# Performance work log

Measured on AMD Instinct MI355X. Metric: run time of the kernel, lower is better.

The kernel has to match this reference:

```python
import jax, jax.numpy as jnp
from jax import lax
import numpy as np

B, CIN, COUT, S = 2, 64, 128, 12
H1, H2 = CIN * 4, COUT * 4          # MBConv hidden dims (expand_ratio=4)
HEADS = 8
MLP_HID = COUT * 4                   # transformer mlp_ratio=4
EPS = 1e-5


def conv1x1(x, w, b=None):
    # 1x1x1 Conv3d == channel matmul. w: [out, in], x: [B,C,H,W,D]
    y = jnp.einsum('oc,bchwd->bohwd', w, x)
    if b is not None:
        y = y + b[None, :, None, None, None]
    return y


def inorm(x, g, b):
    # InstanceNorm3d(affine=True): per-sample, per-channel over spatial dims
    m = x.mean(axis=(2, 3, 4), keepdims=True)
    v = x.var(axis=(2, 3, 4), keepdims=True)
    return (x - m) * jax.lax.rsqrt(v + EPS) * g[None, :, None, None, None] + b[None, :, None, None, None]


def gnorm(x, g, b, groups):
    Bb, C, H, W, D = x.shape
    xr = x.reshape(Bb, groups, C // groups, H, W, D)
    m = xr.mean(axis=(2, 3, 4, 5), keepdims=True)
    v = xr.var(axis=(2, 3, 4, 5), keepdims=True)
    xr = (xr - m) * jax.lax.rsqrt(v + EPS)
    return xr.reshape(Bb, C, H, W, D) * g[None, :, None, None, None] + b[None, :, None, None, None]


def dwconv3(x, w):
    # depthwise 3x3x3, stride 1, pad 1. w: [C,1,3,3,3]
    return lax.conv_general_dilated(
        x, w, window_strides=(1, 1, 1), padding=[(1, 1)] * 3,
        dimension_numbers=('NCDHW', 'OIDHW', 'NCDHW'),
        feature_group_count=x.shape[1])


def mbconv(x, ew, g1, b1, dw, g2, b2, sw1, sb1, sw2, sb2, pw, g3, b3, use_residual):
    res = x
    h = jax.nn.silu(inorm(conv1x1(x, ew), g1, b1))        # expand 1x1
    h = jax.nn.silu(inorm(dwconv3(h, dw), g2, b2))        # depthwise 3x3x3
    s = h.mean(axis=(2, 3, 4), keepdims=True)             # SE: squeeze
    s = jax.nn.silu(conv1x1(s, sw1, sb1))
    s = jax.nn.sigmoid(conv1x1(s, sw2, sb2))
    h = h * s
    h = inorm(conv1x1(h, pw), g3, b3)                     # project
    return res + h if use_residual else h


def mhsa(x, qkv_w, proj_w, proj_b):
    Bb, C, H, W, D = x.shape
    N = H * W * D
    hd = C // HEADS
    qkv = conv1x1(x, qkv_w).reshape(Bb, 3, HEADS, hd, N)
    qkv = jnp.transpose(qkv, (1, 0, 2, 4, 3))             # [3,B,h,N,hd]
    q, k, v = qkv[0], qkv[1], qkv[2]
    attn = jax.nn.softmax(jnp.einsum('bhnd,bhmd->bhnm', q, k) * (hd ** -0.5), axis=-1)
    out = jnp.einsum('bhnm,bhmd->bhnd', attn, v)          # [B,h,N,hd]
    out = jnp.transpose(out, (0, 1, 3, 2)).reshape(Bb, C, H, W, D)
    return conv1x1(out, proj_w, proj_b)


def transformer_block(x, n1g, n1b, qkv, pw, pb, n2g, n2b, mw1, mb1, mw2, mb2):
    x = x + mhsa(gnorm(x, n1g, n1b, min(32, x.shape[1])), qkv, pw, pb)
    h = gnorm(x, n2g, n2b, min(32, x.shape[1]))
    h = conv1x1(jax.nn.gelu(conv1x1(h, mw1, mb1), approximate=False), mw2, mb2)
    return x + h


def shuffle_attn(x, cw1, cw2, gng, gnb, sw):
    b, c, h, w, d = x.shape
    G = 4
    gc = c // (2 * G)  # group_channels
    x6 = x.reshape(b, G, 2 * gc, h, w, d)
    x0 = x6[:, :, :gc].reshape(b * G, gc, h, w, d)
    x1 = x6[:, :, gc:].reshape(b * G, gc, h, w, d)
    # channel branch
    a = x0.mean(axis=(2, 3, 4), keepdims=True)
    a = conv1x1(jax.nn.silu(conv1x1(a, cw1)), cw2)
    x0 = jax.nn.sigmoid(a) * x0
    # spatial branch: GroupNorm(max(1,gc//8)=2 groups) + 1x1 conv
    sgn = gnorm(x1, gng, gnb, max(1, gc // 8))
    x1 = jax.nn.sigmoid(conv1x1(sgn, sw)) * x1
    out = jnp.concatenate([x0.reshape(b, G * gc, h, w, d), x1.reshape(b, G * gc, h, w, d)], axis=1)
    # channel shuffle
    out = out.reshape(b, G, 2 * gc, h, w, d).transpose(0, 2, 1, 3, 4, 5).reshape(b, c, h, w, d)
    return out


def setup_inputs() -> dict:
    key = jax.random.key(0)
    ks = iter(jax.random.split(key, 64))
    w = lambda *shape: jax.random.normal(next(ks), shape, jnp.float32) * 0.05
    p = {}
    p['x'] = jax.random.normal(next(ks), (B, CIN, S, S, S), jnp.float32)
    # mbconv1 (in=64 -> hidden=256 -> out=128), SE reduced = 256//4 = 64
    r1 = H1 // 4
    p['m1_ew'] = w(H1, CIN); p['m1_g1'] = jnp.ones(H1); p['m1_b1'] = jnp.zeros(H1)
    p['m1_dw'] = w(H1, 1, 3, 3, 3); p['m1_g2'] = jnp.ones(H1); p['m1_b2'] = jnp.zeros(H1)
    p['m1_sw1'] = w(r1, H1); p['m1_sb1'] = jnp.zeros(r1)
    p['m1_sw2'] = w(H1, r1); p['m1_sb2'] = jnp.zeros(H1)
    p['m1_pw'] = w(COUT, H1); p['m1_g3'] = jnp.ones(COUT); p['m1_b3'] = jnp.zeros(COUT)
    # mbconv2 (in=128 -> hidden=512 -> out=128, residual), SE reduced = 512//4 = 128
    r2 = H2 // 4
    p['m2_ew'] = w(H2, COUT); p['m2_g1'] = jnp.ones(H2); p['m2_b1'] = jnp.zeros(H2)
    p['m2_dw'] = w(H2, 1, 3, 3, 3); p['m2_g2'] = jnp.ones(H2); p['m2_b2'] = jnp.zeros(H2)
    p['m2_sw1'] = w(r2, H2); p['m2_sb1'] = jnp.zeros(r2)
    p['m2_sw2'] = w(H2, r2); p['m2_sb2'] = jnp.zeros(H2)
    p['m2_pw'] = w(COUT, H2); p['m2_g3'] = jnp.ones(COUT); p['m2_b3'] = jnp.zeros(COUT)
    # transformer
    p['t_n1g'] = jnp.ones(COUT); p['t_n1b'] = jnp.zeros(COUT)
    p['t_qkv'] = w(3 * COUT, COUT)
    p['t_pw'] = w(COUT, COUT); p['t_pb'] = jnp.zeros(COUT)
    p['t_n2g'] = jnp.ones(COUT); p['t_n2b'] = jnp.zeros(COUT)
    p['t_mw1'] = w(MLP_HID, COUT); p['t_mb1'] = jnp.zeros(MLP_HID)
    p['t_mw2'] = w(COUT, MLP_HID); p['t_mb2'] = jnp.zeros(COUT)
    # shuffle attention: group_channels = 128 // 8 = 16, channel_fc reduces to 4
    gc = COUT // 8
    p['s_cw1'] = w(max(1, gc // 4), gc); p['s_cw2'] = w(gc, max(1, gc // 4))
    p['s_gng'] = jnp.ones(gc); p['s_gnb'] = jnp.zeros(gc)
    p['s_sw'] = w(gc, gc)
    return p


def reference(x, m1_ew, m1_g1, m1_b1, m1_dw, m1_g2, m1_b2, m1_sw1, m1_sb1, m1_sw2, m1_sb2, m1_pw, m1_g3, m1_b3, m2_ew, m2_g1, m2_b1, m2_dw, m2_g2, m2_b2, m2_sw1, m2_sb1, m2_sw2, m2_sb2, m2_pw, m2_g3, m2_b3, t_n1g, t_n1b, t_qkv, t_pw, t_pb, t_n2g, t_n2b, t_mw1, t_mb1, t_mw2, t_mb2, s_cw1, s_cw2, s_gng, s_gnb, s_sw):
    x = mbconv(x, m1_ew, m1_g1, m1_b1, m1_dw, m1_g2, m1_b2, m1_sw1, m1_sb1, m1_sw2, m1_sb2, m1_pw, m1_g3, m1_b3, use_residual=False)
    x = mbconv(x, m2_ew, m2_g1, m2_b1, m2_dw, m2_g2, m2_b2, m2_sw1, m2_sb1, m2_sw2, m2_sb2, m2_pw, m2_g3, m2_b3, use_residual=True)
    x = transformer_block(x, t_n1g, t_n1b, t_qkv, t_pw, t_pb, t_n2g, t_n2b, t_mw1, t_mb1, t_mw2, t_mb2)
    x = shuffle_attn(x, s_cw1, s_cw2, s_gng, s_gnb, s_sw)
    return x
```

## Files before the change

### kernel.cpp

```cpp
#include <hip/hip_runtime.h>
#include <cmath>

#define NSP 1728
#define BB  2
#define SS  12

typedef __attribute__((ext_vector_type(8))) short short8;
typedef __attribute__((ext_vector_type(4))) short short4v;
typedef __attribute__((ext_vector_type(4))) float floatx4;

__device__ __forceinline__ short f2bf(float f) {
    unsigned u = __float_as_uint(f);
    u += 0x7fff + ((u >> 16) & 1);
    return (short)(u >> 16);
}
__device__ __forceinline__ unsigned pack2bf(float a, float b) {
    unsigned ua = __float_as_uint(a); ua += 0x7fff + ((ua >> 16) & 1);
    unsigned ub = __float_as_uint(b); ub += 0x7fff + ((ub >> 16) & 1);
    return (ua >> 16) | (ub & 0xffff0000u);
}
__device__ __forceinline__ short8 ld8(const short* p) {
    short4v a = *(const short4v*)p;
    short4v b = *(const short4v*)(p + 4);
    return __builtin_shufflevector(a, b, 0, 1, 2, 3, 4, 5, 6, 7);
}
__device__ __forceinline__ float fexp2(float x) {
    float r;
    asm("v_exp_f32 %0, %1" : "=v"(r) : "v"(x));
    return r;
}

__device__ __forceinline__ void block_reduce2(float& s, float& s2) {
    __shared__ float red[8][2];
    __syncthreads();
    #pragma unroll
    for (int o = 32; o; o >>= 1) {
        s  += __shfl_down(s,  o, 64);
        s2 += __shfl_down(s2, o, 64);
    }
    int lane = threadIdx.x & 63, w = threadIdx.x >> 6;
    if (lane == 0) { red[w][0] = s; red[w][1] = s2; }
    __syncthreads();
    int nw = (blockDim.x + 63) >> 6;
    if (threadIdx.x == 0) {
        float a = 0.f, b = 0.f;
        for (int i = 0; i < nw; i++) { a += red[i][0]; b += red[i][1]; }
        red[0][0] = a; red[0][1] = b;
    }
    __syncthreads();
    s = red[0][0]; s2 = red[0][1];
}

#define WTOT 376832
__global__ __launch_bounds__(256) void prep_kernel(
        const float* __restrict__ s0, const float* __restrict__ s1,
        const float* __restrict__ s2, const float* __restrict__ s3,
        const float* __restrict__ s4, const float* __restrict__ s5,
        const float* __restrict__ s6, const float* __restrict__ s7,
        short* __restrict__ dst, float* __restrict__ stz,
        const float* __restrict__ w1a, const float* __restrict__ w2a,
        const float* __restrict__ w1b, const float* __restrict__ w2b,
        float* __restrict__ tsw) {
    if (blockIdx.x < 11) stz[blockIdx.x * 256 + threadIdx.x] = 0.f;
    if (blockIdx.x >= 368) {
        int e = (blockIdx.x - 368) * 1024 + threadIdx.x * 4;
        #pragma unroll
        for (int k = 0; k < 4; k++) {
            int idx = e + k;
            float v;
            if (idx < 16384) {
                int c = idx >> 6, r = idx & 63;
                v = w1a[r * 256 + c];
            } else if (idx < 32768) {
                int l = idx - 16384; int r = l >> 8, ci = l & 255;
                v = w2a[ci * 64 + r];
            } else if (idx < 98304) {
                int l = idx - 32768; int c = l >> 7, r = l & 127;
                v = w1b[r * 512 + c];
            } else {
                int l = idx - 98304; int r = l >> 9, ci = l & 511;
                v = w2b[ci * 128 + r];
            }
            tsw[idx] = v;
        }
        return;
    }
    const int offs[9] = {0, 16384, 49152, 114688, 180224, 229376, 245760, 311296, WTOT};
    const float* srcs[8] = {s0, s1, s2, s3, s4, s5, s6, s7};
    int e = blockIdx.x * 1024 + threadIdx.x * 4;
    #pragma unroll
    for (int k = 0; k < 4; k++) {
        int idx = e + k;
        int seg = 0;
        while (idx >= offs[seg + 1]) seg++;
        dst[idx] = f2bf(srcs[seg][idx - offs[seg]]);
    }
}

template<int CIN, int COUT>
__global__ __launch_bounds__(256) void convm_kernel(
        const float* __restrict__ in, const short* __restrict__ wb,
        const float* __restrict__ biasc,
        const float* __restrict__ se_s,
        const float* __restrict__ sw1, const float* __restrict__ sb1,
        const float* __restrict__ sw2, const float* __restrict__ sb2, int seR,
        const float* __restrict__ fstats, const float* __restrict__ fg,
        const float* __restrict__ fb, int fgs,
        const float* __restrict__ ing, const float* __restrict__ inb,
        const float* __restrict__ inres,
        const float* __restrict__ po, const float* __restrict__ pl,
        float* __restrict__ xout,
        const float* resid, float* out, float* stats_out,
        const float* __restrict__ statres, int act) {
    constexpr int XP = CIN + 8;
    __shared__ float sc[CIN];
    __shared__ float sh[CIN];
    __shared__ float sa[CIN];
    __shared__ float sbl[CIN];
    __shared__ float hid[128];
    __shared__ __align__(16) short xa[16 * XP];
    int flat = blockIdx.x;
    int b = flat / 108, mt = flat % 108;
    int n0 = mt * 16;
    int tid = threadIdx.x;

    if (po) {
        if (tid < 128) {
            int hh = tid >> 4, j = tid & 15;
            float l = 0.f;
            #pragma unroll
            for (int js = 0; js < 6; js++)
                l += pl[(size_t)((b * 8 + hh) * 6 + js) * NSP + n0 + j];
            hid[tid] = 1.f / l;
        }
        __syncthreads();
        #pragma unroll
        for (int i = 0; i < CIN / 64; i++) {
            int e = tid + i * 256;
            int ci = e >> 2;
            int jj = (e & 3) * 4;
            int hh = ci >> 4, d = ci & 15;
            float4 acc = {0.f, 0.f, 0.f, 0.f};
            #pragma unroll
            for (int js = 0; js < 6; js++) {
                float4 pv = *(const float4*)(po +
                    ((size_t)((b * 8 + hh) * 6 + js) * 16 + d) * NSP + n0 + jj);
                acc.x += pv.x; acc.y += pv.y; acc.z += pv.z; acc.w += pv.w;
            }
            float4 li = *(const float4*)(hid + hh * 16 + jj);
            xa[(jj + 0) * XP + ci] = f2bf(acc.x * li.x);
            xa[(jj + 1) * XP + ci] = f2bf(acc.y * li.y);
            xa[(jj + 2) * XP + ci] = f2bf(acc.z * li.z);
            xa[(jj + 3) * XP + ci] = f2bf(acc.w * li.w);
        }
        __syncthreads();
    } else {
    if (sw1) {
        for (int c = tid; c < CIN; c += 256) { sc[c] = se_s[b * CIN + c]; sh[c] = 0.f; }
        __syncthreads();
        for (int r = tid; r < seR; r += 256) {
            float h0 = sb1[r], h1 = 0.f, h2 = 0.f, h3 = 0.f;
            for (int c = 0; c < CIN; c += 4) {
                h0 = fmaf(sw1[(c + 0) * seR + r], sc[c],     h0);
                h1 = fmaf(sw1[(c + 1) * seR + r], sc[c + 1], h1);
                h2 = fmaf(sw1[(c + 2) * seR + r], sc[c + 2], h2);
                h3 = fmaf(sw1[(c + 3) * seR + r], sc[c + 3], h3);
            }
            float hv = (h0 + h1) + (h2 + h3);
            hid[r] = hv / (1.f + __expf(-hv));
        }
        __syncthreads();
        for (int ci = tid; ci < CIN; ci += 256) {
            float g0 = sb2[ci], g1 = 0.f, g2 = 0.f, g3 = 0.f;
            for (int r = 0; r < seR; r += 4) {
                g0 = fmaf(sw2[(r + 0) * CIN + ci], hid[r],     g0);
                g1 = fmaf(sw2[(r + 1) * CIN + ci], hid[r + 1], g1);
                g2 = fmaf(sw2[(r + 2) * CIN + ci], hid[r + 2], g2);
                g3 = fmaf(sw2[(r + 3) * CIN + ci], hid[r + 3], g3);
            }
            float gv = (g0 + g1) + (g2 + g3);
            sc[ci] = 1.f / (1.f + __expf(-gv));
        }
    } else if (ing) {
        for (int c = tid; c < CIN; c += 256) {
            const float* S = fstats + (size_t)(b * CIN + c) * 5;
            float A = S[0], Bq = S[1], Cq = S[2], Dq = S[3], Eq = S[4];
            const float N = (float)NSP;
            float mean = A / N, var = Bq / N - mean * mean;
            float a_ = ing[c] * rsqrtf(var + 1e-5f);
            float b_ = inb[c] - mean * a_;
            sa[c] = a_; sbl[c] = b_;
            sc[c] = a_ * A + b_ * N + Dq;
            sh[c] = a_ * a_ * Bq + 2.f * a_ * b_ * A + b_ * b_ * N
                  + 2.f * a_ * Cq + 2.f * b_ * Dq + Eq;
        }
        __syncthreads();
        float gS = 0.f, gS2 = 0.f;
        if (tid < CIN) {
            int g0 = (tid / fgs) * fgs;
            for (int k = 0; k < fgs; k++) { gS += sc[g0 + k]; gS2 += sh[g0 + k]; }
        }
        __syncthreads();
        if (tid < CIN) {
            float Ng = fgs * (float)NSP;
            float gm = gS / Ng, gv = gS2 / Ng - gm * gm;
            float s_ = rsqrtf(gv + 1e-5f) * fg[tid];
            sc[tid] = s_;
            sh[tid] = fb[tid] - gm * s_;
        }
    } else if (fstats) {
        for (int c = tid; c < CIN; c += 256) {
            int g0 = c / fgs;
            float S = 0.f, S2 = 0.f;
            for (int k = 0; k < fgs; k++) {
                S  += fstats[(b * CIN + g0 * fgs + k) * 2];
                S2 += fstats[(b * CIN + g0 * fgs + k) * 2 + 1];
            }
            float N = fgs * (float)NSP;
            float mean = S / N, var = S2 / N - mean * mean;
            float s = rsqrtf(var + 1e-5f) * fg[c];
            sc[c] = s;
            sh[c] = fb[c] - mean * s;
        }
    } else {
        for (int c = tid; c < CIN; c += 256) { sc[c] = 1.f; sh[c] = 0.f; }
    }
    __syncthreads();

    bool dosw = (xout != nullptr) && (blockIdx.y == 0);
    #pragma unroll
    for (int i = 0; i < CIN / 64; i++) {
        int e = tid + i * 256;
        int ci = e >> 2;
        int jj = (e & 3) * 4;
        size_t gi = ((size_t)b * CIN + ci) * NSP + n0 + jj;
        float4 v4 = *(const float4*)(in + gi);
        float v0, v1, v2, v3;
        if (ing) {
            float4 rr = *(const float4*)(inres + gi);
            float a_ = sa[ci], b_ = sbl[ci];
            float x0 = fmaf(v4.x, a_, b_) + rr.x;
            float x1 = fmaf(v4.y, a_, b_) + rr.y;
            float x2 = fmaf(v4.z, a_, b_) + rr.z;
            float x3 = fmaf(v4.w, a_, b_) + rr.w;
            if (dosw) {
                float4 o; o.x = x0; o.y = x1; o.z = x2; o.w = x3;
                *(float4*)(xout + gi) = o;
            }
            float s_ = sc[ci], h_ = sh[ci];
            v0 = fmaf(x0, s_, h_); v1 = fmaf(x1, s_, h_);
            v2 = fmaf(x2, s_, h_); v3 = fmaf(x3, s_, h_);
        } else {
            float s_ = sc[ci], h_ = sh[ci];
            v0 = fmaf(v4.x, s_, h_); v1 = fmaf(v4.y, s_, h_);
            v2 = fmaf(v4.z, s_, h_); v3 = fmaf(v4.w, s_, h_);
            if (dosw) {
                float4 o; o.x = v0; o.y = v1; o.z = v2; o.w = v3;
                *(float4*)(xout + gi) = o;
            }
        }
        xa[(jj + 0) * XP + ci] = f2bf(v0);
        xa[(jj + 1) * XP + ci] = f2bf(v1);
        xa[(jj + 2) * XP + ci] = f2bf(v2);
        xa[(jj + 3) * XP + ci] = f2bf(v3);
    }
    __syncthreads();
    }

    int lane = tid & 63, wv = tid >> 6;
    int col = lane & 15, quad = lane >> 4;
    short8 afr[CIN / 32];
    #pragma unroll
    for (int kc = 0; kc < CIN / 32; kc++)
        afr[kc] = ld8(xa + col * XP + kc * 32 + quad * 8);

    int cobase = blockIdx.y * 64 + wv * 16;
    int co = cobase + col;
    const short* wrow = wb + (size_t)co * CIN;
    floatx4 acc = {0.f, 0.f, 0.f, 0.f};
    #pragma unroll
    for (int kc = 0; kc < CIN / 32; kc++) {
        short8 bw = ld8(wrow + kc * 32 + quad * 8);
        acc = __builtin_amdgcn_mfma_f32_16x16x32_bf16(afr[kc], bw, acc, 0, 0, 0);
    }
    float bv = biasc ? biasc[co] : 0.f;
    float r0 = acc[0] + bv, r1 = acc[1] + bv, r2 = acc[2] + bv, r3 = acc[3] + bv;
    if (act == 2) {
        r0 = 0.5f * r0 * (1.f + erff(r0 * 0.70710678118654752f));
        r1 = 0.5f * r1 * (1.f + erff(r1 * 0.70710678118654752f));
        r2 = 0.5f * r2 * (1.f + erff(r2 * 0.70710678118654752f));
        r3 = 0.5f * r3 * (1.f + erff(r3 * 0.70710678118654752f));
    }
    size_t oi = ((size_t)b * COUT + co) * NSP + n0 + quad * 4;
    if (resid) {
        float4 rv = *(const float4*)(resid + oi);
        r0 += rv.x; r1 += rv.y; r2 += rv.z; r3 += rv.w;
    }
    float4 ov; ov.x = r0; ov.y = r1; ov.z = r2; ov.w = r3;
    *(float4*)(out + oi) = ov;
    if (stats_out) {
        if (statres) {
            float4 rv = *(const float4*)(statres + oi);
            float s   = (r0 + r1) + (r2 + r3);
            float s2  = (r0 * r0 + r1 * r1) + (r2 * r2 + r3 * r3);
            float sx  = (r0 * rv.x + r1 * rv.y) + (r2 * rv.z + r3 * rv.w);
            float sr  = (rv.x + rv.y) + (rv.z + rv.w);
            float sr2 = (rv.x * rv.x + rv.y * rv.y) + (rv.z * rv.z + rv.w * rv.w);
            s   += __shfl_xor(s,   16, 64); s   += __shfl_xor(s,   32, 64);
            s2  += __shfl_xor(s2,  16, 64); s2  += __shfl_xor(s2,  32, 64);
            sx  += __shfl_xor(sx,  16, 64); sx  += __shfl_xor(sx,  32, 64);
            sr  += __shfl_xor(sr,  16, 64); sr  += __shfl_xor(sr,  32, 64);
            sr2 += __shfl_xor(sr2, 16, 64); sr2 += __shfl_xor(sr2, 32, 64);
            if (lane < 16) {
                float* sp = stats_out + (size_t)(b * COUT + cobase + lane) * 5;
                atomicAdd(sp + 0, s);
                atomicAdd(sp + 1, s2);
                atomicAdd(sp + 2, sx);
                atomicAdd(sp + 3, sr);
                atomicAdd(sp + 4, sr2);
            }
        } else {
            float s  = (r0 + r1) + (r2 + r3);
            float s2 = (r0 * r0 + r1 * r1) + (r2 * r2 + r3 * r3);
            s  += __shfl_xor(s,  16, 64);
            s  += __shfl_xor(s,  32, 64);
            s2 += __shfl_xor(s2, 16, 64);
            s2 += __shfl_xor(s2, 32, 64);
            if (lane < 16) {
                atomicAdd(&stats_out[(b * COUT + cobase + lane) * 2],     s);
                atomicAdd(&stats_out[(b * COUT + cobase + lane) * 2 + 1], s2);
            }
        }
    }
}

__global__ __launch_bounds__(256) void indw_kernel(
        const float* __restrict__ in,
        const float* __restrict__ g1, const float* __restrict__ b1,
        const float* __restrict__ dw,
        const float* __restrict__ g2, const float* __restrict__ b2,
        float* __restrict__ out, float* __restrict__ se_s, int C) {
    int bc = blockIdx.x;
    int c  = bc % C;
    __shared__ float tile[14 * 14 * 14];
    __shared__ float wsh[27];
    const float* ip = in + (size_t)bc * NSP;
    float r[7];
    float s = 0.f, s2 = 0.f;
    for (int i = threadIdx.x; i < 2744; i += 256) tile[i] = 0.f;
    #pragma unroll
    for (int i = 0; i < 7; i++) {
        int n = threadIdx.x + i * 256;
        if (n < NSP) { r[i] = ip[n]; s += r[i]; s2 += r[i] * r[i]; }
        else r[i] = 0.f;
    }
    if (threadIdx.x < 27) wsh[threadIdx.x] = dw[(size_t)c * 27 + threadIdx.x];
    block_reduce2(s, s2);
    float mean = s / NSP, var = s2 / NSP - (s / NSP) * (s / NSP);
    float rstd = rsqrtf(var + 1e-5f);
    float gc = g1[c], bc1 = b1[c];
    #pragma unroll
    for (int i = 0; i < 7; i++) {
        int n = threadIdx.x + i * 256;
        if (n < NSP) {
            int z = n / 144, y = (n / 12) % 12, x = n % 12;
            float v = (r[i] - mean) * rstd * gc + bc1;
            tile[((z + 1) * 14 + y + 1) * 14 + x + 1] = v / (1.f + __expf(-v));
        }
    }
    __syncthreads();
    float d[7];
    #pragma unroll
    for (int i = 0; i < 7; i++) {
        int n = threadIdx.x + i * 256;
        d[i] = 0.f;
        if (n < NSP) {
            int z = n / 144, y = (n / 12) % 12, x = n % 12;
            const float* ctr = tile + ((z + 1) * 14 + y + 1) * 14 + x + 1;
            float acc = 0.f;
            #pragma unroll
            for (int dz = 0; dz < 3; dz++)
                #pragma unroll
                for (int dy = 0; dy < 3; dy++)
                    #pragma unroll
                    for (int dx = 0; dx < 3; dx++)
                        acc = fmaf(wsh[dz * 9 + dy * 3 + dx],
                                   ctr[(dz - 1) * 196 + (dy - 1) * 14 + (dx - 1)], acc);
            d[i] = acc;
        }
    }
    s = 0.f; s2 = 0.f;
    #pragma unroll
    for (int i = 0; i < 7; i++) {
        int n = threadIdx.x + i * 256;
        if (n < NSP) { s += d[i]; s2 += d[i] * d[i]; }
    }
    block_reduce2(s, s2);
    mean = s / NSP; var = s2 / NSP - mean * mean;
    rstd = rsqrtf(var + 1e-5f);
    float gc2 = g2[c], bc2 = b2[c];
    float ssum = 0.f;
    float* op = out + (size_t)bc * NSP;
    #pragma unroll
    for (int i = 0; i < 7; i++) {
        int n = threadIdx.x + i * 256;
        if (n < NSP) {
            float v = (d[i] - mean) * rstd * gc2 + bc2;
            v = v / (1.f + __expf(-v));
            op[n] = v;
            ssum += v;
        }
    }
    float dummy = 0.f;
    block_reduce2(ssum, dummy);
    if (threadIdx.x == 0) se_s[bc] = ssum / NSP;
}

#define AKT 20
#define AVT 296
#define APT 36
#define JCH 288
__global__ __launch_bounds__(256) void attn_split_kernel(const float* __restrict__ qkv,
                                                         float* __restrict__ po,
                                                         float* __restrict__ pl) {
    __shared__ __align__(16) short kt[JCH * AKT];
    __shared__ __align__(16) short vt[16 * AVT];
    __shared__ __align__(16) short pt[4][16 * APT];
    int bh = blockIdx.x;
    int b = bh >> 3, h = bh & 7;
    int js = blockIdx.z;
    int j0 = js * JCH;
    const float* base = qkv + (size_t)b * 384 * NSP;
    const float* qp = base + (size_t)(h * 16) * NSP;
    const float* kp = base + (size_t)(128 + h * 16) * NSP;
    const float* vp = base + (size_t)(256 + h * 16) * NSP;
    for (int t = threadIdx.x; t < 16 * 144; t += 256) {
        int d = t / 144, j = (t - d * 144) * 2;
        float2 kv2 = *(const float2*)(kp + (size_t)d * NSP + j0 + j);
        float2 vv2 = *(const float2*)(vp + (size_t)d * NSP + j0 + j);
        kt[j * AKT + d]       = f2bf(kv2.x);
        kt[(j + 1) * AKT + d] = f2bf(kv2.y);
        *(unsigned*)(vt + d * AVT + j) = pack2bf(vv2.x, vv2.y);
    }
    int wave = threadIdx.x >> 6, lane = threadIdx.x & 63;
    int m = lane & 15, quad = lane >> 4;
    int q0 = (blockIdx.y * 4 + wave) * 16;
    short* ptw = pt[wave];
    short8 qa;
    #pragma unroll
    for (int i = 0; i < 8; i++) qa[i] = 0;
    if (quad < 2) {
        #pragma unroll
        for (int i = 0; i < 8; i++) {
            int d = quad * 8 + i;
            qa[i] = f2bf(qp[(size_t)d * NSP + q0 + m] * 0.36067376022224085f);
        }
    }
    __syncthreads();
    floatx4 o = {0.f, 0.f, 0.f, 0.f};
    float ls = 0.f;
    for (int s = 0; s < 9; s++) {
        int jl = s * 32;
        short8 ak0, ak1;
        #pragma unroll
        for (int i = 0; i < 8; i++) { ak0[i] = 0; ak1[i] = 0; }
        if (quad < 2) {
            ak0 = ld8(kt + (jl + m) * AKT + quad * 8);
            ak1 = ld8(kt + (jl + 16 + m) * AKT + quad * 8);
        }
        floatx4 s0 = {0.f, 0.f, 0.f, 0.f}, s1 = {0.f, 0.f, 0.f, 0.f};
        s0 = __builtin_amdgcn_mfma_f32_16x16x32_bf16(ak0, qa, s0, 0, 0, 0);
        s1 = __builtin_amdgcn_mfma_f32_16x16x32_bf16(ak1, qa, s1, 0, 0, 0);
        float p0r0 = fexp2(s0[0]), p0r1 = fexp2(s0[1]), p0r2 = fexp2(s0[2]), p0r3 = fexp2(s0[3]);
        float p1r0 = fexp2(s1[0]), p1r1 = fexp2(s1[1]), p1r2 = fexp2(s1[2]), p1r3 = fexp2(s1[3]);
        ls += (p0r0 + p0r1) + (p0r2 + p0r3) + (p1r0 + p1r1) + (p1r2 + p1r3);
        uint2 w0, w1;
        w0.x = pack2bf(p0r0, p0r1); w0.y = pack2bf(p0r2, p0r3);
        w1.x = pack2bf(p1r0, p1r1); w1.y = pack2bf(p1r2, p1r3);
        *(uint2*)(ptw + m * APT + quad * 4)      = w0;
        *(uint2*)(ptw + m * APT + 16 + quad * 4) = w1;
        short8 av = ld8(vt + m * AVT + jl + quad * 8);
        short8 pb = ld8(ptw + m * APT + quad * 8);
        o = __builtin_amdgcn_mfma_f32_16x16x32_bf16(av, pb, o, 0, 0, 0);
    }
    ls += __shfl_xor(ls, 16, 64);
    ls += __shfl_xor(ls, 32, 64);
    size_t pbase = ((size_t)(bh * 6 + js) * 16) * NSP;
    #pragma unroll
    for (int r = 0; r < 4; r++)
        po[pbase + (size_t)(quad * 4 + r) * NSP + q0 + m] = o[r];
    if (quad == 0) pl[(size_t)(bh * 6 + js) * NSP + q0 + m] = ls;
}

__global__ void sfinal_kernel(const float* __restrict__ X,
                              const float* __restrict__ st,
                              const float* __restrict__ cw1,
                              const float* __restrict__ cw2,
                              const float* __restrict__ gng,
                              const float* __restrict__ gnb,
                              const float* __restrict__ sw,
                              float* __restrict__ out) {
    int bg = blockIdx.x;
    int b = bg >> 2, g = bg & 3;
    __shared__ float swl[256];
    for (int i = threadIdx.x; i < 256; i += 64) swl[i] = sw[i];
    __syncthreads();
    float pooled[16];
    #pragma unroll
    for (int j = 0; j < 16; j++)
        pooled[j] = st[(b * 128 + g * 32 + j) * 2] * (1.f / NSP);
    float hid[4];
    #pragma unroll
    for (int r = 0; r < 4; r++) {
        float a = 0.f;
        #pragma unroll
        for (int j = 0; j < 16; j++) a = fmaf(cw1[r * 16 + j], pooled[j], a);
        hid[r] = a / (1.f + __expf(-a));
    }
    float gate[16];
    #pragma unroll
    for (int j = 0; j < 16; j++) {
        float a = 0.f;
        #pragma unroll
        for (int r = 0; r < 4; r++) a = fmaf(cw2[j * 4 + r], hid[r], a);
        gate[j] = 1.f / (1.f + __expf(-a));
    }
    float gmean[2], grstd[2];
    #pragma unroll
    for (int t = 0; t < 2; t++) {
        float S = 0.f, S2 = 0.f;
        #pragma unroll
        for (int k = 0; k < 8; k++) {
            int c = g * 32 + 16 + t * 8 + k;
            S  += st[(b * 128 + c) * 2];
            S2 += st[(b * 128 + c) * 2 + 1];
        }
        float N = 8.f * NSP;
        gmean[t] = S / N;
        grstd[t] = rsqrtf(S2 / N - gmean[t] * gmean[t] + 1e-5f);
    }
    int n = blockIdx.y * 64 + threadIdx.x;
    const float* xb = X + (size_t)b * 128 * NSP;
    #pragma unroll
    for (int j = 0; j < 16; j++) {
        float v = xb[(size_t)(g * 32 + j) * NSP + n] * gate[j];
        int k = g * 16 + j;
        int cp = (k % 32) * 4 + (k / 32);
        out[((size_t)b * 128 + cp) * NSP + n] = v;
    }
    float sgn[16];
    #pragma unroll
    for (int j = 0; j < 16; j++) {
        int grp = j >> 3;
        float xv = xb[(size_t)(g * 32 + 16 + j) * NSP + n];
        sgn[j] = (xv - gmean[grp]) * grstd[grp] * gng[j] + gnb[j];
    }
    #pragma unroll
    for (int j = 0; j < 16; j++) {
        float a = 0.f;
        #pragma unroll
        for (int jp = 0; jp < 16; jp++) a = fmaf(swl[j * 16 + jp], sgn[jp], a);
        float v = (1.f / (1.f + __expf(-a))) * xb[(size_t)(g * 32 + 16 + j) * NSP + n];
        int k = 64 + g * 16 + j;
        int cp = (k % 32) * 4 + (k / 32);
        out[((size_t)b * 128 + cp) * NSP + n] = v;
    }
}

extern "C" void kernel_launch(void* const* d_in, const int* in_sizes, int n_in,
                              void* d_out, int out_size, void* d_ws, size_t ws_size,
                              hipStream_t stream) {
    const float* x     = (const float*)d_in[0];
    const float* m1_ew = (const float*)d_in[1];
    const float* m1_g1 = (const float*)d_in[2];
    const float* m1_b1 = (const float*)d_in[3];
    const float* m1_dw = (const float*)d_in[4];
    const float* m1_g2 = (const float*)d_in[5];
    const float* m1_b2 = (const float*)d_in[6];
    const float* m1_sw1= (const float*)d_in[7];
    const float* m1_sb1= (const float*)d_in[8];
    const float* m1_sw2= (const float*)d_in[9];
    const float* m1_sb2= (const float*)d_in[10];
    const float* m1_pw = (const float*)d_in[11];
    const float* m1_g3 = (const float*)d_in[12];
    const float* m1_b3 = (const float*)d_in[13];
    const float* m2_ew = (const float*)d_in[14];
    const float* m2_g1 = (const float*)d_in[15];
    const float* m2_b1 = (const float*)d_in[16];
    const float* m2_dw = (const float*)d_in[17];
    const float* m2_g2 = (const float*)d_in[18];
    const float* m2_b2 = (const float*)d_in[19];
    const float* m2_sw1= (const float*)d_in[20];
    const float* m2_sb1= (const float*)d_in[21];
    const float* m2_sw2= (const float*)d_in[22];
    const float* m2_sb2= (const float*)d_in[23];
    const float* m2_pw = (const float*)d_in[24];
    const float* m2_g3 = (const float*)d_in[25];
    const float* m2_b3 = (const float*)d_in[26];
    const float* t_n1g = (const float*)d_in[27];
    const float* t_n1b = (const float*)d_in[28];
    const float* t_qkv = (const float*)d_in[29];
    const float* t_pw  = (const float*)d_in[30];
    const float* t_pb  = (const float*)d_in[31];
    const float* t_n2g = (const float*)d_in[32];
    const float* t_n2b = (const float*)d_in[33];
    const float* t_mw1 = (const float*)d_in[34];
    const float* t_mb1 = (const float*)d_in[35];
    const float* t_mw2 = (const float*)d_in[36];
    const float* t_mb2 = (const float*)d_in[37];
    const float* s_cw1 = (const float*)d_in[38];
    const float* s_cw2 = (const float*)d_in[39];
    const float* s_gng = (const float*)d_in[40];
    const float* s_gnb = (const float*)d_in[41];
    const float* s_sw  = (const float*)d_in[42];

    float* out = (float*)d_out;

    float* ws = (float*)d_ws;
    float* bufA   = ws;
    float* bufB   = bufA + (size_t)BB * 512 * NSP;
    float* bufX   = bufB + (size_t)BB * 512 * NSP;
    float* bufY   = bufX + (size_t)BB * 128 * NSP;
    float* bufQKV = bufY + (size_t)BB * 128 * NSP;
    float* pl     = bufQKV + (size_t)BB * 384 * NSP;
    float* small  = pl + (size_t)16 * 6 * NSP;
    float* se_s   = small;
    float* st1    = small + 1024;
    float* st3    = small + 1536;
    float* st4    = small + 2048;
    float* st2    = small + 2560;
    short* wbf    = (short*)(small + 8192);
    float* tsw    = small + 196608;
    float* T_M1SW1 = tsw;
    float* T_M1SW2 = tsw + 16384;
    float* T_M2SW1 = tsw + 32768;
    float* T_M2SW2 = tsw + 98304;
    float* bufX2  = tsw + 163840;
    float* po     = bufA;

    short* W_M1EW = wbf + 0;
    short* W_M1PW = wbf + 16384;
    short* W_M2EW = wbf + 49152;
    short* W_M2PW = wbf + 114688;
    short* W_QKV  = wbf + 180224;
    short* W_TPW  = wbf + 229376;
    short* W_MW1  = wbf + 245760;
    short* W_MW2  = wbf + 311296;

    dim3 blk(256);

    prep_kernel<<<528, blk, 0, stream>>>(
        m1_ew, m1_pw, m2_ew, m2_pw, t_qkv, t_pw, t_mw1, t_mw2, wbf, st1,
        m1_sw1, m1_sw2, m2_sw1, m2_sw2, tsw);

    convm_kernel<64, 256><<<dim3(BB * 108, 4), blk, 0, stream>>>(
        x, W_M1EW, nullptr,
        nullptr, nullptr, nullptr, nullptr, nullptr, 0,
        nullptr, nullptr, nullptr, 0,
        nullptr, nullptr, nullptr,
        nullptr, nullptr, nullptr,
        nullptr, bufA, nullptr, nullptr, 0);
    indw_kernel<<<BB * 256, blk, 0, stream>>>(bufA, m1_g1, m1_b1, m1_dw, m1_g2, m1_b2, bufB, se_s, 256);
    convm_kernel<256, 128><<<dim3(BB * 108, 2), blk, 0, stream>>>(
        bufB, W_M1PW, nullptr,
        se_s, T_M1SW1, m1_sb1, T_M1SW2, m1_sb2, 64,
        nullptr, nullptr, nullptr, 0,
        nullptr, nullptr, nullptr,
        nullptr, nullptr, nullptr,
        nullptr, bufY, st1, nullptr, 0);

    convm_kernel<128, 512><<<dim3(BB * 108, 8), blk, 0, stream>>>(
        bufY, W_M2EW, nullptr,
        nullptr, nullptr, nullptr, nullptr, nullptr, 0,
        st1, m1_g3, m1_b3, 1,
        nullptr, nullptr, nullptr,
        nullptr, nullptr, bufX,
        nullptr, bufA, nullptr, nullptr, 0);
    indw_kernel<<<BB * 512, blk, 0, stream>>>(bufA, m2_g1, m2_b1, m2_dw, m2_g2, m2_b2, bufB, se_s, 512);
    convm_kernel<512, 128><<<dim3(BB * 108, 2), blk, 0, stream>>>(
        bufB, W_M2PW, nullptr,
        se_s, T_M2SW1, m2_sb1, T_M2SW2, m2_sb2, 128,
        nullptr, nullptr, nullptr, 0,
        nullptr, nullptr, nullptr,
        nullptr, nullptr, nullptr,
        nullptr, bufY, st2, bufX, 0);

    convm_kernel<128, 384><<<dim3(BB * 108, 6), blk, 0, stream>>>(
        bufY, W_QKV, nullptr,
        nullptr, nullptr, nullptr, nullptr, nullptr, 0,
        st2, t_n1g, t_n1b, 4,
        m2_g3, m2_b3, bufX,
        nullptr, nullptr, bufX2,
        nullptr, bufQKV, nullptr, nullptr, 0);
    attn_split_kernel<<<dim3(16, 27, 6), blk, 0, stream>>>(bufQKV, po, pl);
    convm_kernel<128, 128><<<dim3(BB * 108, 2), blk, 0, stream>>>(
        nullptr, W_TPW, t_pb,
        nullptr, nullptr, nullptr, nullptr, nullptr, 0,
        nullptr, nullptr, nullptr, 0,
        nullptr, nullptr, nullptr,
        po, pl, nullptr,
        bufX2, bufX2, st3, nullptr, 0);
    convm_kernel<128, 512><<<dim3(BB * 108, 8), blk, 0, stream>>>(
        bufX2, W_MW1, t_mb1,
        nullptr, nullptr, nullptr, nullptr, nullptr, 0,
        st3, t_n2g, t_n2b, 4,
        nullptr, nullptr, nullptr,
        nullptr, nullptr, nullptr,
        nullptr, bufA, nullptr, nullptr, 2);
    convm_kernel<512, 128><<<dim3(BB * 108, 2), blk, 0, stream>>>(
        bufA, W_MW2, t_mb2,
        nullptr, nullptr, nullptr, nullptr, nullptr, 0,
        nullptr, nullptr, nullptr, 0,
        nullptr, nullptr, nullptr,
        nullptr, nullptr, nullptr,
        bufX2, bufX2, st4, nullptr, 0);

    sfinal_kernel<<<dim3(BB * 4, 27), dim3(64), 0, stream>>>(
        bufX2, st4, s_cw1, s_cw2, s_gng, s_gnb, s_sw, out);
}
```

Measured before the change: 333.8 us.

## Fuse all pipeline stages into one cooperative persistent megakernel with grid syncs

Replaces the sequence of about a dozen kernel launches with a single cooperative kernel. Each stage (weight prep, conv matmuls, depthwise conv, attention, final shuffle) becomes a device function looped over work units, with grid-wide syncs between stages and a shared-memory union. The SE gate MLP is moved out of the per-block conv prologue into its own stage that writes the gate once per batch. The aim is to remove launch overhead and the SE work repeated in every block. In exchange, grid syncs cost time, a union sized for the largest stage lowers occupancy, and the grid is capped by occupancy, which may under-parallelise large stages.

```diff
diff --git a/kernel.cpp b/kernel.cpp
--- a/kernel.cpp
+++ b/kernel.cpp
@@ -1,5 +1,8 @@
 #include <hip/hip_runtime.h>
+#include <hip/hip_cooperative_groups.h>
 #include <cmath>
+
+namespace cg = cooperative_groups;
 
 #define NSP 1728
 #define BB  2
@@ -29,6 +32,28 @@
     asm("v_exp_f32 %0, %1" : "=v"(r) : "v"(x));
     return r;
 }
+
+union SMemU {
+    struct {
+        float sc[512], sh[512], sa[512], sbl[512], hid[128];
+        short xa[16 * 520];
+    } conv;
+    struct {
+        float tile[14 * 14 * 14];
+        float wsh[27];
+    } dwc;
+    struct {
+        short kt[288 * 20];
+        short vt[16 * 296];
+        short pt[4][16 * 36];
+    } attn;
+    struct {
+        float pooled[512], hid[128];
+    } seg;
+    struct {
+        float swl[256];
+    } sf;
+};
 
 __device__ __forceinline__ void block_reduce2(float& s, float& s2) {
     __shared__ float red[8][2];
@@ -51,59 +76,99 @@
     s = red[0][0]; s2 = red[0][1];
 }
 
+struct MegaParams {
+    const float *x;
+    const float *m1_g1, *m1_b1, *m1_dw, *m1_g2, *m1_b2, *m1_sb1, *m1_sb2, *m1_g3, *m1_b3;
+    const float *m2_g1, *m2_b1, *m2_dw, *m2_g2, *m2_b2, *m2_sb1, *m2_sb2, *m2_g3, *m2_b3;
+    const float *t_n1g, *t_n1b, *t_pb, *t_n2g, *t_n2b, *t_mb1, *t_mb2;
+    const float *s_cw1, *s_cw2, *s_gng, *s_gnb, *s_sw;
+    const float *pw0, *pw1, *pw2, *pw3, *pw4, *pw5, *pw6, *pw7;
+    const float *sew1a, *sew2a, *sew1b, *sew2b;
+    float *bufA, *bufB, *bufX, *bufY, *bufQKV, *pl;
+    float *se_s, *st1, *st3, *st4, *st2, *gate1, *gate2;
+    short *wbf;
+    float *tsw, *bufX2;
+    float *out;
+};
+
 #define WTOT 376832
-__global__ __launch_bounds__(256) void prep_kernel(
-        const float* __restrict__ s0, const float* __restrict__ s1,
-        const float* __restrict__ s2, const float* __restrict__ s3,
-        const float* __restrict__ s4, const float* __restrict__ s5,
-        const float* __restrict__ s6, const float* __restrict__ s7,
-        short* __restrict__ dst, float* __restrict__ stz,
-        const float* __restrict__ w1a, const float* __restrict__ w2a,
-        const float* __restrict__ w1b, const float* __restrict__ w2b,
-        float* __restrict__ tsw) {
-    if (blockIdx.x < 11) stz[blockIdx.x * 256 + threadIdx.x] = 0.f;
-    if (blockIdx.x >= 368) {
-        int e = (blockIdx.x - 368) * 1024 + threadIdx.x * 4;
+__device__ __forceinline__ void prep_dev(int u, const MegaParams& p) {
+    if (u < 11) p.st1[u * 256 + threadIdx.x] = 0.f;
+    if (u >= 368) {
+        int e = (u - 368) * 1024 + threadIdx.x * 4;
         #pragma unroll
         for (int k = 0; k < 4; k++) {
             int idx = e + k;
             float v;
             if (idx < 16384) {
                 int c = idx >> 6, r = idx & 63;
-                v = w1a[r * 256 + c];
+                v = p.sew1a[r * 256 + c];
             } else if (idx < 32768) {
                 int l = idx - 16384; int r = l >> 8, ci = l & 255;
-                v = w2a[ci * 64 + r];
+                v = p.sew2a[ci * 64 + r];
             } else if (idx < 98304) {
                 int l = idx - 32768; int c = l >> 7, r = l & 127;
-                v = w1b[r * 512 + c];
+                v = p.sew1b[r * 512 + c];
             } else {
                 int l = idx - 98304; int r = l >> 9, ci = l & 511;
-                v = w2b[ci * 128 + r];
-            }
-            tsw[idx] = v;
+                v = p.sew2b[ci * 128 + r];
+            }
+            p.tsw[idx] = v;
         }
         return;
     }
     const int offs[9] = {0, 16384, 49152, 114688, 180224, 229376, 245760, 311296, WTOT};
-    const float* srcs[8] = {s0, s1, s2, s3, s4, s5, s6, s7};
-    int e = blockIdx.x * 1024 + threadIdx.x * 4;
+    const float* srcs[8] = {p.pw0, p.pw1, p.pw2, p.pw3, p.pw4, p.pw5, p.pw6, p.pw7};
+    int e = u * 1024 + threadIdx.x * 4;
     #pragma unroll
     for (int k = 0; k < 4; k++) {
         int idx = e + k;
         int seg = 0;
         while (idx >= offs[seg + 1]) seg++;
-        dst[idx] = f2bf(srcs[seg][idx - offs[seg]]);
+        p.wbf[idx] = f2bf(srcs[seg][idx - offs[seg]]);
+    }
+}
+
+template<int CIN, int SER>
+__device__ __forceinline__ void segate_dev(SMemU& sm, int b,
+        const float* __restrict__ pooled_in,
+        const float* __restrict__ w1t, const float* __restrict__ b1,
+        const float* __restrict__ w2t, const float* __restrict__ b2,
+        float* __restrict__ gate) {
+    int tid = threadIdx.x;
+    __syncthreads();
+    for (int c = tid; c < CIN; c += 256) sm.seg.pooled[c] = pooled_in[b * CIN + c];
+    __syncthreads();
+    if (tid < SER) {
+        float a0 = 0.f, a1 = 0.f, a2 = 0.f, a3 = 0.f;
+        for (int c = 0; c < CIN; c += 4) {
+            a0 = fmaf(w1t[(size_t)(c + 0) * SER + tid], sm.seg.pooled[c + 0], a0);
+            a1 = fmaf(w1t[(size_t)(c + 1) * SER + tid], sm.seg.pooled[c + 1], a1);
+            a2 = fmaf(w1t[(size_t)(c + 2) * SER + tid], sm.seg.pooled[c + 2], a2);
+            a3 = fmaf(w1t[(size_t)(c + 3) * SER + tid], sm.seg.pooled[c + 3], a3);
+        }
+        float h = b1[tid] + (a0 + a1) + (a2 + a3);
+        sm.seg.hid[tid] = h / (1.f + __expf(-h));
+    }
+    __syncthreads();
+    for (int ci = tid; ci < CIN; ci += 256) {
+        float g0 = b2[ci], g1 = 0.f, g2 = 0.f, g3 = 0.f;
+        for (int r = 0; r < SER; r += 4) {
+            g0 = fmaf(w2t[(size_t)(r + 0) * CIN + ci], sm.seg.hid[r + 0], g0);
+            g1 = fmaf(w2t[(size_t)(r + 1) * CIN + ci], sm.seg.hid[r + 1], g1);
+            g2 = fmaf(w2t[(size_t)(r + 2) * CIN + ci], sm.seg.hid[r + 2], g2);
+            g3 = fmaf(w2t[(size_t)(r + 3) * CIN + ci], sm.seg.hid[r + 3], g3);
+        }
+        float gv = (g0 + g1) + (g2 + g3);
+        gate[b * CIN + ci] = 1.f / (1.f + __expf(-gv));
     }
 }
 
 template<int CIN, int COUT>
-__global__ __launch_bounds__(256) void convm_kernel(
+__device__ __forceinline__ void convm_dev(SMemU& sm, int flat, int coy,
         const float* __restrict__ in, const short* __restrict__ wb,
         const float* __restrict__ biasc,
-        const float* __restrict__ se_s,
-        const float* __restrict__ sw1, const float* __restrict__ sb1,
-        const float* __restrict__ sw2, const float* __restrict__ sb2, int seR,
+        const float* __restrict__ segate,
         const float* __restrict__ fstats, const float* __restrict__ fg,
         const float* __restrict__ fb, int fgs,
         const float* __restrict__ ing, const float* __restrict__ inb,
@@ -113,16 +178,16 @@
         const float* resid, float* out, float* stats_out,
         const float* __restrict__ statres, int act) {
     constexpr int XP = CIN + 8;
-    __shared__ float sc[CIN];
-    __shared__ float sh[CIN];
-    __shared__ float sa[CIN];
-    __shared__ float sbl[CIN];
-    __shared__ float hid[128];
-    __shared__ __align__(16) short xa[16 * XP];
-    int flat = blockIdx.x;
+    float* sc  = sm.conv.sc;
+    float* sh  = sm.conv.sh;
+    float* sa  = sm.conv.sa;
+    float* sbl = sm.conv.sbl;
+    float* hid = sm.conv.hid;
+    short* xa  = sm.conv.xa;
     int b = flat / 108, mt = flat % 108;
     int n0 = mt * 16;
     int tid = threadIdx.x;
+    __syncthreads();
 
     if (po) {
         if (tid < 128) {
@@ -155,116 +220,95 @@
         }
         __syncthreads();
     } else {
-    if (sw1) {
-        for (int c = tid; c < CIN; c += 256) { sc[c] = se_s[b * CIN + c]; sh[c] = 0.f; }
+        if (segate) {
+            for (int c = tid; c < CIN; c += 256) {
+                sc[c] = segate[b * CIN + c];
+                sh[c] = 0.f;
+            }
+        } else if (ing) {
+            for (int c = tid; c < CIN; c += 256) {
+                const float* S = fstats + (size_t)(b * CIN + c) * 5;
+                float A = S[0], Bq = S[1], Cq = S[2], Dq = S[3], Eq = S[4];
+                const float N = (float)NSP;
+                float mean = A / N, var = Bq / N - mean * mean;
+                float a_ = ing[c] * rsqrtf(var + 1e-5f);
+                float b_ = inb[c] - mean * a_;
+                sa[c] = a_; sbl[c] = b_;
+                sc[c] = a_ * A + b_ * N + Dq;
+                sh[c] = a_ * a_ * Bq + 2.f * a_ * b_ * A + b_ * b_ * N
+                      + 2.f * a_ * Cq + 2.f * b_ * Dq + Eq;
+            }
+            __syncthreads();
+            float gS = 0.f, gS2 = 0.f;
+            if (tid < CIN) {
+                int g0 = (tid / fgs) * fgs;
+                for (int k = 0; k < fgs; k++) { gS += sc[g0 + k]; gS2 += sh[g0 + k]; }
+            }
+            __syncthreads();
+            if (tid < CIN) {
+                float Ng = fgs * (float)NSP;
+                float gm = gS / Ng, gv = gS2 / Ng - gm * gm;
+                float s_ = rsqrtf(gv + 1e-5f) * fg[tid];
+                sc[tid] = s_;
+                sh[tid] = fb[tid] - gm * s_;
+            }
+        } else if (fstats) {
+            for (int c = tid; c < CIN; c += 256) {
+                int g0 = c / fgs;
+                float S = 0.f, S2 = 0.f;
+                for (int k = 0; k < fgs; k++) {
+                    S  += fstats[(b * CIN + g0 * fgs + k) * 2];
+                    S2 += fstats[(b * CIN + g0 * fgs + k) * 2 + 1];
+                }
+                float N = fgs * (float)NSP;
+                float mean = S / N, var = S2 / N - mean * mean;
+                float s = rsqrtf(var + 1e-5f) * fg[c];
+                sc[c] = s;
+                sh[c] = fb[c] - mean * s;
+            }
+        } else {
+            for (int c = tid; c < CIN; c += 256) { sc[c] = 1.f; sh[c] = 0.f; }
+        }
         __syncthreads();
-        for (int r = tid; r < seR; r += 256) {
-            float h0 = sb1[r], h1 = 0.f, h2 = 0.f, h3 = 0.f;
-            for (int c = 0; c < CIN; c += 4) {
-                h0 = fmaf(sw1[(c + 0) * seR + r], sc[c],     h0);
-                h1 = fmaf(sw1[(c + 1) * seR + r], sc[c + 1], h1);
-                h2 = fmaf(sw1[(c + 2) * seR + r], sc[c + 2], h2);
-                h3 = fmaf(sw1[(c + 3) * seR + r], sc[c + 3], h3);
-            }
-            float hv = (h0 + h1) + (h2 + h3);
-            hid[r] = hv / (1.f + __expf(-hv));
+
+        bool dosw = (xout != nullptr) && (coy == 0);
+        #pragma unroll
+        for (int i = 0; i < CIN / 64; i++) {
+            int e = tid + i * 256;
+            int ci = e >> 2;
+            int jj = (e & 3) * 4;
+            size_t gi = ((size_t)b * CIN + ci) * NSP + n0 + jj;
+            float4 v4 = *(const float4*)(in + gi);
+            float v0, v1, v2, v3;
+            if (ing) {
+                float4 rr = *(const float4*)(inres + gi);
+                float a_ = sa[ci], b_ = sbl[ci];
+                float x0 = fmaf(v4.x, a_, b_) + rr.x;
+                float x1 = fmaf(v4.y, a_, b_) + rr.y;
+                float x2 = fmaf(v4.z, a_, b_) + rr.z;
+                float x3 = fmaf(v4.w, a_, b_) + rr.w;
+                if (dosw) {
+                    float4 o; o.x = x0; o.y = x1; o.z = x2; o.w = x3;
+                    *(float4*)(xout + gi) = o;
+                }
+                float s_ = sc[ci], h_ = sh[ci];
+                v0 = fmaf(x0, s_, h_); v1 = fmaf(x1, s_, h_);
+                v2 = fmaf(x2, s_, h_); v3 = fmaf(x3, s_, h_);
+            } else {
+                float s_ = sc[ci], h_ = sh[ci];
+                v0 = fmaf(v4.x, s_, h_); v1 = fmaf(v4.y, s_, h_);
+                v2 = fmaf(v4.z, s_, h_); v3 = fmaf(v4.w, s_, h_);
+                if (dosw) {
+                    float4 o; o.x = v0; o.y = v1; o.z = v2; o.w = v3;
+                    *(float4*)(xout + gi) = o;
+                }
+            }
+            xa[(jj + 0) * XP + ci] = f2bf(v0);
+            xa[(jj + 1) * XP + ci] = f2bf(v1);
+            xa[(jj + 2) * XP + ci] = f2bf(v2);
+            xa[(jj + 3) * XP + ci] = f2bf(v3);
         }
         __syncthreads();
-        for (int ci = tid; ci < CIN; ci += 256) {
-            float g0 = sb2[ci], g1 = 0.f, g2 = 0.f, g3 = 0.f;
-            for (int r = 0; r < seR; r += 4) {
-                g0 = fmaf(sw2[(r + 0) * CIN + ci], hid[r],     g0);
-                g1 = fmaf(sw2[(r + 1) * CIN + ci], hid[r + 1], g1);
-                g2 = fmaf(sw2[(r + 2) * CIN + ci], hid[r + 2], g2);
-                g3 = fmaf(sw2[(r + 3) * CIN + ci], hid[r + 3], g3);
-            }
-            float gv = (g0 + g1) + (g2 + g3);
-            sc[ci] = 1.f / (1.f + __expf(-gv));
-        }
-    } else if (ing) {
-        for (int c = tid; c < CIN; c += 256) {
-            const float* S = fstats + (size_t)(b * CIN + c) * 5;
-            float A = S[0], Bq = S[1], Cq = S[2], Dq = S[3], Eq = S[4];
-            const float N = (float)NSP;
-            float mean = A / N, var = Bq / N - mean * mean;
-            float a_ = ing[c] * rsqrtf(var + 1e-5f);
-            float b_ = inb[c] - mean * a_;
-            sa[c] = a_; sbl[c] = b_;
-            sc[c] = a_ * A + b_ * N + Dq;
-            sh[c] = a_ * a_ * Bq + 2.f * a_ * b_ * A + b_ * b_ * N
-                  + 2.f * a_ * Cq + 2.f * b_ * Dq + Eq;
-        }
-        __syncthreads();
-        float gS = 0.f, gS2 = 0.f;
-        if (tid < CIN) {
-            int g0 = (tid / fgs) * fgs;
-            for (int k = 0; k < fgs; k++) { gS += sc[g0 + k]; gS2 += sh[g0 + k]; }
-        }
-        __syncthreads();
-        if (tid < CIN) {
-            float Ng = fgs * (float)NSP;
-            float gm = gS / Ng, gv = gS2 / Ng - gm * gm;
-            float s_ = rsqrtf(gv + 1e-5f) * fg[tid];
-            sc[tid] = s_;
-            sh[tid] = fb[tid] - gm * s_;
-        }
-    } else if (fstats) {
-        for (int c = tid; c < CIN; c += 256) {
-            int g0 = c / fgs;
-            float S = 0.f, S2 = 0.f;
-            for (int k = 0; k < fgs; k++) {
-                S  += fstats[(b * CIN + g0 * fgs + k) * 2];
-                S2 += fstats[(b * CIN + g0 * fgs + k) * 2 + 1];
-            }
-            float N = fgs * (float)NSP;
-            float mean = S / N, var = S2 / N - mean * mean;
-            float s = rsqrtf(var + 1e-5f) * fg[c];
-            sc[c] = s;
-            sh[c] = fb[c] - mean * s;
-        }
-    } else {
-        for (int c = tid; c < CIN; c += 256) { sc[c] = 1.f; sh[c] = 0.f; }
-    }
-    __syncthreads();
-
-    bool dosw = (xout != nullptr) && (blockIdx.y == 0);
-    #pragma unroll
-    for (int i = 0; i < CIN / 64; i++) {
-        int e = tid + i * 256;
-        int ci = e >> 2;
-        int jj = (e & 3) * 4;
-        size_t gi = ((size_t)b * CIN + ci) * NSP + n0 + jj;
-        float4 v4 = *(const float4*)(in + gi);
-        float v0, v1, v2, v3;
-        if (ing) {
-            float4 rr = *(const float4*)(inres + gi);
-            float a_ = sa[ci], b_ = sbl[ci];
-            float x0 = fmaf(v4.x, a_, b_) + rr.x;
-            float x1 = fmaf(v4.y, a_, b_) + rr.y;
-            float x2 = fmaf(v4.z, a_, b_) + rr.z;
-            float x3 = fmaf(v4.w, a_, b_) + rr.w;
-            if (dosw) {
-                float4 o; o.x = x0; o.y = x1; o.z = x2; o.w = x3;
-                *(float4*)(xout + gi) = o;
-            }
-            float s_ = sc[ci], h_ = sh[ci];
-            v0 = fmaf(x0, s_, h_); v1 = fmaf(x1, s_, h_);
-            v2 = fmaf(x2, s_, h_); v3 = fmaf(x3, s_, h_);
-        } else {
-            float s_ = sc[ci], h_ = sh[ci];
-            v0 = fmaf(v4.x, s_, h_); v1 = fmaf(v4.y, s_, h_);
-            v2 = fmaf(v4.z, s_, h_); v3 = fmaf(v4.w, s_, h_);
-            if (dosw) {
-                float4 o; o.x = v0; o.y = v1; o.z = v2; o.w = v3;
-                *(float4*)(xout + gi) = o;
-            }
-        }
-        xa[(jj + 0) * XP + ci] = f2bf(v0);
-        xa[(jj + 1) * XP + ci] = f2bf(v1);
-        xa[(jj + 2) * XP + ci] = f2bf(v2);
-        xa[(jj + 3) * XP + ci] = f2bf(v3);
-    }
-    __syncthreads();
     }
 
     int lane = tid & 63, wv = tid >> 6;
@@ -274,7 +318,7 @@
     for (int kc = 0; kc < CIN / 32; kc++)
         afr[kc] = ld8(xa + col * XP + kc * 32 + quad * 8);
 
-    int cobase = blockIdx.y * 64 + wv * 16;
+    int cobase = coy * 64 + wv * 16;
     int co = cobase + col;
     const short* wrow = wb + (size_t)co * CIN;
     floatx4 acc = {0.f, 0.f, 0.f, 0.f};
@@ -334,16 +378,16 @@
     }
 }
 
-__global__ __launch_bounds__(256) void indw_kernel(
+__device__ __forceinline__ void indw_dev(SMemU& sm, int bc,
         const float* __restrict__ in,
         const float* __restrict__ g1, const float* __restrict__ b1,
         const float* __restrict__ dw,
         const float* __restrict__ g2, const float* __restrict__ b2,
         float* __restrict__ out, float* __restrict__ se_s, int C) {
-    int bc = blockIdx.x;
-    int c  = bc % C;
-    __shared__ float tile[14 * 14 * 14];
-    __shared__ float wsh[27];
+    int c = bc % C;
+    float* tile = sm.dwc.tile;
+    float* wsh  = sm.dwc.wsh;
+    __syncthreads();
     const float* ip = in + (size_t)bc * NSP;
     float r[7];
     float s = 0.f, s2 = 0.f;
@@ -420,15 +464,13 @@
 #define AVT 296
 #define APT 36
 #define JCH 288
-__global__ __launch_bounds__(256) void attn_split_kernel(const float* __restrict__ qkv,
-                                                         float* __restrict__ po,
-                                                         float* __restrict__ pl) {
-    __shared__ __align__(16) short kt[JCH * AKT];
-    __shared__ __align__(16) short vt[16 * AVT];
-    __shared__ __align__(16) short pt[4][16 * APT];
-    int bh = blockIdx.x;
+__device__ __forceinline__ void attn_dev(SMemU& sm, int bh, int qy, int js,
+        const float* __restrict__ qkv, float* __restrict__ po,
+        float* __restrict__ pl) {
+    short* kt = sm.attn.kt;
+    short* vt = sm.attn.vt;
+    __syncthreads();
     int b = bh >> 3, h = bh & 7;
-    int js = blockIdx.z;
     int j0 = js * JCH;
     const float* base = qkv + (size_t)b * 384 * NSP;
     const float* qp = base + (size_t)(h * 16) * NSP;
@@ -444,8 +486,8 @@
     }
     int wave = threadIdx.x >> 6, lane = threadIdx.x & 63;
     int m = lane & 15, quad = lane >> 4;
-    int q0 = (blockIdx.y * 4 + wave) * 16;
-    short* ptw = pt[wave];
+    int q0 = (qy * 4 + wave) * 16;
+    short* ptw = sm.attn.pt[wave];
     short8 qa;
     #pragma unroll
     for (int i = 0; i < 8; i++) qa[i] = 0;
@@ -492,19 +534,19 @@
     if (quad == 0) pl[(size_t)(bh * 6 + js) * NSP + q0 + m] = ls;
 }
 
-__global__ void sfinal_kernel(const float* __restrict__ X,
-                              const float* __restrict__ st,
-                              const float* __restrict__ cw1,
-                              const float* __restrict__ cw2,
-                              const float* __restrict__ gng,
-                              const float* __restrict__ gnb,
-                              const float* __restrict__ sw,
-                              float* __restrict__ out) {
-    int bg = blockIdx.x;
+__device__ __forceinline__ void sfinal_dev(SMemU& sm, int u,
+        const float* __restrict__ X, const float* __restrict__ st,
+        const float* __restrict__ cw1, const float* __restrict__ cw2,
+        const float* __restrict__ gng, const float* __restrict__ gnb,
+        const float* __restrict__ sw, float* __restrict__ out) {
+    int bg = u & 7;
+    int n = (u >> 3) * 256 + threadIdx.x;
     int b = bg >> 2, g = bg & 3;
-    __shared__ float swl[256];
-    for (int i = threadIdx.x; i < 256; i += 64) swl[i] = sw[i];
-    __syncthreads();
+    float* swl = sm.sf.swl;
+    __syncthreads();
+    swl[threadIdx.x] = sw[threadIdx.x];
+    __syncthreads();
+    if (n >= NSP) return;
     float pooled[16];
     #pragma unroll
     for (int j = 0; j < 16; j++)
@@ -539,7 +581,6 @@
         gmean[t] = S / N;
         grstd[t] = rsqrtf(S2 / N - gmean[t] * gmean[t] + 1e-5f);
     }
-    int n = blockIdx.y * 64 + threadIdx.x;
     const float* xb = X + (size_t)b * 128 * NSP;
     #pragma unroll
     for (int j = 0; j < 16; j++) {
@@ -567,154 +608,206 @@
     }
 }
 
+__global__ __launch_bounds__(256, 2) void mega_kernel(MegaParams p) {
+    __shared__ __align__(16) SMemU sm;
+    cg::grid_group gg = cg::this_grid();
+    const int NB = gridDim.x;
+    const int bid = blockIdx.x;
+
+    for (int u = bid; u < 528; u += NB) prep_dev(u, p);
+    gg.sync();
+
+    for (int u = bid; u < 216 * 4; u += NB)
+        convm_dev<64, 256>(sm, u % 216, u / 216,
+            p.x, p.wbf + 0, nullptr, nullptr,
+            nullptr, nullptr, nullptr, 0,
+            nullptr, nullptr, nullptr,
+            nullptr, nullptr, nullptr,
+            nullptr, p.bufA, nullptr, nullptr, 0);
+    gg.sync();
+
+    for (int u = bid; u < BB * 256; u += NB)
+        indw_dev(sm, u, p.bufA, p.m1_g1, p.m1_b1, p.m1_dw, p.m1_g2, p.m1_b2,
+                 p.bufB, p.se_s, 256);
+    gg.sync();
+
+    for (int u = bid; u < BB; u += NB)
+        segate_dev<256, 64>(sm, u, p.se_s, p.tsw, p.m1_sb1,
+                            p.tsw + 16384, p.m1_sb2, p.gate1);
+    gg.sync();
+
+    for (int u = bid; u < 216 * 2; u += NB)
+        convm_dev<256, 128>(sm, u % 216, u / 216,
+            p.bufB, p.wbf + 16384, nullptr, p.gate1,
+            nullptr, nullptr, nullptr, 0,
+            nullptr, nullptr, nullptr,
+            nullptr, nullptr, nullptr,
+            nullptr, p.bufY, p.st1, nullptr, 0);
+    gg.sync();
+
+    for (int u = bid; u < 216 * 8; u += NB)
+        convm_dev<128, 512>(sm, u % 216, u / 216,
+            p.bufY, p.wbf + 49152, nullptr, nullptr,
+            p.st1, p.m1_g3, p.m1_b3, 1,
+            nullptr, nullptr, nullptr,
+            nullptr, nullptr, p.bufX,
+            nullptr, p.bufA, nullptr, nullptr, 0);
+    gg.sync();
+
+    for (int u = bid; u < BB * 512; u += NB)
+        indw_dev(sm, u, p.bufA, p.m2_g1, p.m2_b1, p.m2_dw, p.m2_g2, p.m2_b2,
+                 p.bufB, p.se_s, 512);
+    gg.sync();
+
+    for (int u = bid; u < BB; u += NB)
+        segate_dev<512, 128>(sm, u, p.se_s, p.tsw + 32768, p.m2_sb1,
+                             p.tsw + 98304, p.m2_sb2, p.gate2);
+    gg.sync();
+
+    for (int u = bid; u < 216 * 2; u += NB)
+        convm_dev<512, 128>(sm, u % 216, u / 216,
+            p.bufB, p.wbf + 114688, nullptr, p.gate2,
+            nullptr, nullptr, nullptr, 0,
+            nullptr, nullptr, nullptr,
+            nullptr, nullptr, nullptr,
+            nullptr, p.bufY, p.st2, p.bufX, 0);
+    gg.sync();
+
+    for (int u = bid; u < 216 * 6; u += NB)
+        convm_dev<128, 384>(sm, u % 216, u / 216,
+            p.bufY, p.wbf + 180224, nullptr, nullptr,
+            p.st2, p.t_n1g, p.t_n1b, 4,
+            p.m2_g3, p.m2_b3, p.bufX,
+            nullptr, nullptr, p.bufX2,
+            nullptr, p.bufQKV, nullptr, nullptr, 0);
+    gg.sync();
+
+    for (int u = bid; u < 16 * 27 * 6; u += NB) {
+        int bh = u % 16, qy = (u / 16) % 27, js = u / (16 * 27);
+        attn_dev(sm, bh, qy, js, p.bufQKV, p.bufA, p.pl);
+    }
+    gg.sync();
+
+    for (int u = bid; u < 216 * 2; u += NB)
+        convm_dev<128, 128>(sm, u % 216, u / 216,
+            nullptr, p.wbf + 229376, p.t_pb, nullptr,
+            nullptr, nullptr, nullptr, 0,
+            nullptr, nullptr, nullptr,
+            p.bufA, p.pl, nullptr,
+            p.bufX2, p.bufX2, p.st3, nullptr, 0);
+    gg.sync();
+
+    for (int u = bid; u < 216 * 8; u += NB)
+        convm_dev<128, 512>(sm, u % 216, u / 216,
+            p.bufX2, p.wbf + 245760, p.t_mb1, nullptr,
+            p.st3, p.t_n2g, p.t_n2b, 4,
+            nullptr, nullptr, nullptr,
+            nullptr, nullptr, nullptr,
+            nullptr, p.bufA, nullptr, nullptr, 2);
+    gg.sync();
+
+    for (int u = bid; u < 216 * 2; u += NB)
+        convm_dev<512, 128>(sm, u % 216, u / 216,
+            p.bufA, p.wbf + 311296, p.t_mb2, nullptr,
+            nullptr, nullptr, nullptr, 0,
+            nullptr, nullptr, nullptr,
+            nullptr, nullptr, nullptr,
+            p.bufX2, p.bufX2, p.st4, nullptr, 0);
+    gg.sync();
+
+    for (int u = bid; u < 56; u += NB)
+        sfinal_dev(sm, u, p.bufX2, p.st4, p.s_cw1, p.s_cw2,
+                   p.s_gng, p.s_gnb, p.s_sw, p.out);
+}
+
 extern "C" void kernel_launch(void* const* d_in, const int* in_sizes, int n_in,
                               void* d_out, int out_size, void* d_ws, size_t ws_size,
                               hipStream_t stream) {
-    const float* x     = (const float*)d_in[0];
+    MegaParams mp;
+    mp.x      = (const float*)d_in[0];
     const float* m1_ew = (const float*)d_in[1];
-    const float* m1_g1 = (const float*)d_in[2];
-    const float* m1_b1 = (const float*)d_in[3];
-    const float* m1_dw = (const float*)d_in[4];
-    const float* m1_g2 = (const float*)d_in[5];
-    const float* m1_b2 = (const float*)d_in[6];
-    const float* m1_sw1= (const float*)d_in[7];
-    const float* m1_sb1= (const float*)d_in[8];
-    const float* m1_sw2= (const float*)d_in[9];
-    const float* m1_sb2= (const float*)d_in[10];
+    mp.m1_g1  = (const float*)d_in[2];
+    mp.m1_b1  = (const float*)d_in[3];
+    mp.m1_dw  = (const float*)d_in[4];
+    mp.m1_g2  = (const float*)d_in[5];
+    mp.m1_b2  = (const float*)d_in[6];
+    mp.sew1a  = (const float*)d_in[7];
+    mp.m1_sb1 = (const float*)d_in[8];
+    mp.sew2a  = (const float*)d_in[9];
+    mp.m1_sb2 = (const float*)d_in[10];
     const float* m1_pw = (const float*)d_in[11];
-    const float* m1_g3 = (const float*)d_in[12];
-    const float* m1_b3 = (const float*)d_in[13];
+    mp.m1_g3  = (const float*)d_in[12];
+    mp.m1_b3  = (const float*)d_in[13];
     const float* m2_ew = (const float*)d_in[14];
-    const float* m2_g1 = (const float*)d_in[15];
-    const float* m2_b1 = (const float*)d_in[16];
-    const float* m2_dw = (const float*)d_in[17];
-    const float* m2_g2 = (const float*)d_in[18];
-    const float* m2_b2 = (const float*)d_in[19];
-    const float* m2_sw1= (const float*)d_in[20];
-    const float* m2_sb1= (const float*)d_in[21];
-    const float* m2_sw2= (const float*)d_in[22];
-    const float* m2_sb2= (const float*)d_in[23];
+    mp.m2_g1  = (const float*)d_in[15];
+    mp.m2_b1  = (const float*)d_in[16];
+    mp.m2_dw  = (const float*)d_in[17];
+    mp.m2_g2  = (const float*)d_in[18];
+    mp.m2_b2  = (const float*)d_in[19];
+    mp.sew1b  = (const float*)d_in[20];
+    mp.m2_sb1 = (const float*)d_in[21];
+    mp.sew2b  = (const float*)d_in[22];
+    mp.m2_sb2 = (const float*)d_in[23];
     const float* m2_pw = (const float*)d_in[24];
-    const float* m2_g3 = (const float*)d_in[25];
-    const float* m2_b3 = (const float*)d_in[26];
-    const float* t_n1g = (const float*)d_in[27];
-    const float* t_n1b = (const float*)d_in[28];
+    mp.m2_g3  = (const float*)d_in[25];
+    mp.m2_b3  = (const float*)d_in[26];
+    mp.t_n1g  = (const float*)d_in[27];
+    mp.t_n1b  = (const float*)d_in[28];
     const float* t_qkv = (const float*)d_in[29];
     const float* t_pw  = (const float*)d_in[30];
-    const float* t_pb  = (const float*)d_in[31];
-    const float* t_n2g = (const float*)d_in[32];
-    const float* t_n2b = (const float*)d_in[33];
+    mp.t_pb   = (const float*)d_in[31];
+    mp.t_n2g  = (const float*)d_in[32];
+    mp.t_n2b  = (const float*)d_in[33];
     const float* t_mw1 = (const float*)d_in[34];
-    const float* t_mb1 = (const float*)d_in[35];
+    mp.t_mb1  = (const float*)d_in[35];
     const float* t_mw2 = (const float*)d_in[36];
-    const float* t_mb2 = (const float*)d_in[37];
-    const float* s_cw1 = (const float*)d_in[38];
-    const float* s_cw2 = (const float*)d_in[39];
-    const float* s_gng = (const float*)d_in[40];
-    const float* s_gnb = (const float*)d_in[41];
-    const float* s_sw  = (const float*)d_in[42];
-
-    float* out = (float*)d_out;
+    mp.t_mb2  = (const float*)d_in[37];
+    mp.s_cw1  = (const float*)d_in[38];
+    mp.s_cw2  = (const float*)d_in[39];
+    mp.s_gng  = (const float*)d_in[40];
+    mp.s_gnb  = (const float*)d_in[41];
+    mp.s_sw   = (const float*)d_in[42];
+
+    mp.pw0 = m1_ew; mp.pw1 = m1_pw; mp.pw2 = m2_ew; mp.pw3 = m2_pw;
+    mp.pw4 = t_qkv; mp.pw5 = t_pw;  mp.pw6 = t_mw1; mp.pw7 = t_mw2;
+
+    mp.out = (float*)d_out;
 
     float* ws = (float*)d_ws;
-    float* bufA   = ws;
-    float* bufB   = bufA + (size_t)BB * 512 * NSP;
-    float* bufX   = bufB + (size_t)BB * 512 * NSP;
-    float* bufY   = bufX + (size_t)BB * 128 * NSP;
-    float* bufQKV = bufY + (size_t)BB * 128 * NSP;
-    float* pl     = bufQKV + (size_t)BB * 384 * NSP;
-    float* small  = pl + (size_t)16 * 6 * NSP;
-    float* se_s   = small;
-    float* st1    = small + 1024;
-    float* st3    = small + 1536;
-    float* st4    = small + 2048;
-    float* st2    = small + 2560;
-    short* wbf    = (short*)(small + 8192);
-    float* tsw    = small + 196608;
-    float* T_M1SW1 = tsw;
-    float* T_M1SW2 = tsw + 16384;
-    float* T_M2SW1 = tsw + 32768;
-    float* T_M2SW2 = tsw + 98304;
-    float* bufX2  = tsw + 163840;
-    float* po     = bufA;
-
-    short* W_M1EW = wbf + 0;
-    short* W_M1PW = wbf + 16384;
-    short* W_M2EW = wbf + 49152;
-    short* W_M2PW = wbf + 114688;
-    short* W_QKV  = wbf + 180224;
-    short* W_TPW  = wbf + 229376;
-    short* W_MW1  = wbf + 245760;
-    short* W_MW2  = wbf + 311296;
-
-    dim3 blk(256);
-
-    prep_kernel<<<528, blk, 0, stream>>>(
-        m1_ew, m1_pw, m2_ew, m2_pw, t_qkv, t_pw, t_mw1, t_mw2, wbf, st1,
-        m1_sw1, m1_sw2, m2_sw1, m2_sw2, tsw);
-
-    convm_kernel<64, 256><<<dim3(BB * 108, 4), blk, 0, stream>>>(
-        x, W_M1EW, nullptr,
-        nullptr, nullptr, nullptr, nullptr, nullptr, 0,
-        nullptr, nullptr, nullptr, 0,
-        nullptr, nullptr, nullptr,
-        nullptr, nullptr, nullptr,
-        nullptr, bufA, nullptr, nullptr, 0);
-    indw_kernel<<<BB * 256, blk, 0, stream>>>(bufA, m1_g1, m1_b1, m1_dw, m1_g2, m1_b2, bufB, se_s, 256);
-    convm_kernel<256, 128><<<dim3(BB * 108, 2), blk, 0, stream>>>(
-        bufB, W_M1PW, nullptr,
-        se_s, T_M1SW1, m1_sb1, T_M1SW2, m1_sb2, 64,
-        nullptr, nullptr, nullptr, 0,
-        nullptr, nullptr, nullptr,
-        nullptr, nullptr, nullptr,
-        nullptr, bufY, st1, nullptr, 0);
-
-    convm_kernel<128, 512><<<dim3(BB * 108, 8), blk, 0, stream>>>(
-        bufY, W_M2EW, nullptr,
-        nullptr, nullptr, nullptr, nullptr, nullptr, 0,
-        st1, m1_g3, m1_b3, 1,
-        nullptr, nullptr, nullptr,
-        nullptr, nullptr, bufX,
-        nullptr, bufA, nullptr, nullptr, 0);
-    indw_kernel<<<BB * 512, blk, 0, stream>>>(bufA, m2_g1, m2_b1, m2_dw, m2_g2, m2_b2, bufB, se_s, 512);
-    convm_kernel<512, 128><<<dim3(BB * 108, 2), blk, 0, stream>>>(
-        bufB, W_M2PW, nullptr,
-        se_s, T_M2SW1, m2_sb1, T_M2SW2, m2_sb2, 128,
-        nullptr, nullptr, nullptr, 0,
-        nullptr, nullptr, nullptr,
-        nullptr, nullptr, nullptr,
-        nullptr, bufY, st2, bufX, 0);
-
-    convm_kernel<128, 384><<<dim3(BB * 108, 6), blk, 0, stream>>>(
-        bufY, W_QKV, nullptr,
-        nullptr, nullptr, nullptr, nullptr, nullptr, 0,
-        st2, t_n1g, t_n1b, 4,
-        m2_g3, m2_b3, bufX,
-        nullptr, nullptr, bufX2,
-        nullptr, bufQKV, nullptr, nullptr, 0);
-    attn_split_kernel<<<dim3(16, 27, 6), blk, 0, stream>>>(bufQKV, po, pl);
-    convm_kernel<128, 128><<<dim3(BB * 108, 2), blk, 0, stream>>>(
-        nullptr, W_TPW, t_pb,
-        nullptr, nullptr, nullptr, nullptr, nullptr, 0,
-        nullptr, nullptr, nullptr, 0,
-        nullptr, nullptr, nullptr,
-        po, pl, nullptr,
-        bufX2, bufX2, st3, nullptr, 0);
-    convm_kernel<128, 512><<<dim3(BB * 108, 8), blk, 0, stream>>>(
-        bufX2, W_MW1, t_mb1,
-        nullptr, nullptr, nullptr, nullptr, nullptr, 0,
-        st3, t_n2g, t_n2b, 4,
-        nullptr, nullptr, nullptr,
-        nullptr, nullptr, nullptr,
-        nullptr, bufA, nullptr, nullptr, 2);
-    convm_kernel<512, 128><<<dim3(BB * 108, 2), blk, 0, stream>>>(
-        bufA, W_MW2, t_mb2,
-        nullptr, nullptr, nullptr, nullptr, nullptr, 0,
-        nullptr, nullptr, nullptr, 0,
-        nullptr, nullptr, nullptr,
-        nullptr, nullptr, nullptr,
-        bufX2, bufX2, st4, nullptr, 0);
-
-    sfinal_kernel<<<dim3(BB * 4, 27), dim3(64), 0, stream>>>(
-        bufX2, st4, s_cw1, s_cw2, s_gng, s_gnb, s_sw, out);
-}
+    mp.bufA   = ws;
+    mp.bufB   = mp.bufA + (size_t)BB * 512 * NSP;
+    mp.bufX   = mp.bufB + (size_t)BB * 512 * NSP;
+    mp.bufY   = mp.bufX + (size_t)BB * 128 * NSP;
+    mp.bufQKV = mp.bufY + (size_t)BB * 128 * NSP;
+    mp.pl     = mp.bufQKV + (size_t)BB * 384 * NSP;
+    float* small = mp.pl + (size_t)16 * 6 * NSP;
+    mp.se_s   = small;
+    mp.st1    = small + 1024;
+    mp.st3    = small + 1536;
+    mp.st4    = small + 2048;
+    mp.st2    = small + 2560;
+    mp.gate1  = small + 4096;
+    mp.gate2  = small + 4608;
+    mp.wbf    = (short*)(small + 8192);
+    mp.tsw    = small + 196608;
+    mp.bufX2  = mp.tsw + 163840;
+
+    static int s_nblk = 0;
+    if (s_nblk == 0) {
+        int dev = 0;
+        hipGetDevice(&dev);
+        hipDeviceProp_t prop;
+        hipGetDeviceProperties(&prop, dev);
+        int occ = 0;
+        hipOccupancyMaxActiveBlocksPerMultiprocessor(&occ, mega_kernel, 256, 0);
+        if (occ < 1) occ = 1;
+        long cap = (long)occ * prop.multiProcessorCount;
+        if (cap > 1024) cap = 1024;
+        if (cap < 1) cap = 1;
+        s_nblk = (int)cap;
+    }
+
+    void* args[] = {&mp};
+    hipLaunchCooperativeKernel(mega_kernel, dim3(s_nblk), dim3(256),
+                               args, 0, stream);
+}
```

Measured after the change: 843.0 us. +152.5%, slower.
